# Performance work log

Measured on AMD Instinct MI355X. Metric: run time of the kernel, lower is better.

## Reference

```python
import jax, jax.numpy as jnp
import numpy as np
from jax import lax

PI = float(np.pi)
K_TOP = 128
N_BINS = 64

def _normalize(x, axis, eps=1e-12):
    n = jnp.sqrt(jnp.sum(x * x, axis=axis, keepdims=True))
    return x / jnp.maximum(n, eps)

def _conv(x, w, b):
    y = lax.conv_general_dilated(x, w, (1, 1), 'SAME',
                                 dimension_numbers=('NCHW', 'OIHW', 'NCHW'))
    return y + b[None, :, None, None]

def _maxpool2(x):
    return lax.reduce_window(x, -jnp.inf, lax.max, (1, 1, 2, 2), (1, 1, 2, 2), 'VALID')

def setup_inputs() -> dict:
    key = jax.random.key(0)
    ks = jax.random.split(key, 12)
    B, C, H, W = 16, 1, 512, 512
    PD, NPT = 128, 64
    fc_in = NPT + 64 * 4 * 4 + 3  # 1091
    def lin_init(k, fan_in, shape):
        bound = 1.0 / np.sqrt(fan_in)
        return jax.random.uniform(k, shape, jnp.float32, -bound, bound)
    return {
        'image': jax.random.normal(ks[0], (B, C, H, W), jnp.float32),
        'pattern_receptors': jax.random.normal(ks[1], (NPT, PD), jnp.float32) * 0.1,
        'conv1_w': lin_init(ks[2], 2 * 9, (32, 2, 3, 3)),
        'conv1_b': lin_init(ks[3], 2 * 9, (32,)),
        'conv2_w': lin_init(ks[4], 32 * 9, (64, 32, 3, 3)),
        'conv2_b': lin_init(ks[5], 32 * 9, (64,)),
        'fc1_w': lin_init(ks[6], fc_in, (512, fc_in)),
        'fc1_b': lin_init(ks[7], fc_in, (512,)),
        'fc2_w': lin_init(ks[8], 512, (PD, 512)),
        'fc2_b': lin_init(ks[9], 512, (PD,)),
        'ln_g': jnp.ones((PD,), jnp.float32),
        'ln_b': jnp.zeros((PD,), jnp.float32),
    }

def reference(image, pattern_receptors, conv1_w, conv1_b, conv2_w, conv2_b,
              fc1_w, fc1_b, fc2_w, fc2_b, ln_g, ln_b):
    B, C, H, W = image.shape
    # ---- frequency domain ----
    freq = jnp.fft.fft2(image, axes=(2, 3))
    magnitude = jnp.abs(freq)
    phase = jnp.angle(freq)
    # ---- pattern matching (topk of FFT magnitude vs receptor library) ----
    flat_mag = magnitude.reshape(B, C, -1)
    dom, _ = lax.top_k(flat_mag, K_TOP)          # [B, C, 128]
    dom = dom.reshape(B, -1)                     # [B, C*128]
    sims = jnp.matmul(_normalize(dom, 1), _normalize(pattern_receptors, 1).T)  # [B, 64]
    # ---- spatial path (original detaches via numpy roundtrip) ----
    img = lax.stop_gradient(image)
    gy = jnp.gradient(img, axis=2)
    gx = jnp.gradient(img, axis=3)
    gmag = jnp.sqrt(gx * gx + gy * gy)
    gori = jnp.arctan2(gy, gx)
    spat_in = jnp.stack([gmag, gori], axis=2).reshape(B, 2 * C, H, W)
    h = jax.nn.relu(_conv(spat_in, conv1_w, conv1_b))
    h = _maxpool2(h)                             # [B,32,H/2,W/2]
    h = jax.nn.relu(_conv(h, conv2_w, conv2_b))  # [B,64,H/2,W/2]
    Hp, Wp = h.shape[2], h.shape[3]
    h = h.reshape(B, 64, 4, Hp // 4, 4, Wp // 4).mean(axis=(3, 5))  # adaptive avg 4x4
    spatial = h.reshape(B, -1)                   # [B, 1024]
    # ---- phase statistics ----
    pf = phase.reshape(B, -1)
    p_mean = jnp.mean(pf, axis=1)
    p_std = jnp.std(pf, axis=1, ddof=1)
    bins = jnp.clip(jnp.floor((pf + PI) / (2 * PI) * N_BINS), 0, N_BINS - 1).astype(jnp.int32)
    hist = jnp.zeros((B, N_BINS), jnp.float32).at[jnp.arange(B)[:, None], bins].add(1.0)
    hist = hist / jnp.sum(hist, axis=1, keepdims=True)
    p_ent = -jnp.sum(hist * jnp.log(hist + 1e-10), axis=1)
    phase_feats = jnp.stack([p_mean, p_std, p_ent], axis=1)  # [B, 3]
    # ---- fuse: MLP + LayerNorm ----
    combined = jnp.concatenate([sims, spatial, phase_feats], axis=1)  # [B, 1091]
    z = jax.nn.relu(combined @ fc1_w.T + fc1_b)
    z = z @ fc2_w.T + fc2_b
    mu = jnp.mean(z, axis=-1, keepdims=True)
    var = jnp.var(z, axis=-1, keepdims=True)
    holo = (z - mu) / jnp.sqrt(var + 1e-5) * ln_g + ln_b
    return sims, spatial, phase_feats, holo
```

## Files before the change

### kernel.cpp

```cpp
#include <hip/hip_runtime.h>
#include <hip/hip_fp16.h>
#include <math.h>


#define PI_F 3.14159274f
#define TWO_PI_F 6.28318548f

typedef _Float16 half8 __attribute__((ext_vector_type(8)));
typedef _Float16 h2 __attribute__((ext_vector_type(2)));
typedef float floatx4 __attribute__((ext_vector_type(4)));

#define OFF_BIG   8388608
#define OFF_SMALL 25165824
#define NBIN 2048

__global__ void __launch_bounds__(256) init_kernel(float* __restrict__ zp,
                                                   float2* __restrict__ tw,
                                                   const float* __restrict__ w2,
                                                   const float* __restrict__ w1,
                                                   _Float16* __restrict__ wrep,
                                                   _Float16* __restrict__ w1r) {
    int idx = blockIdx.x * 256 + threadIdx.x;
    if (idx < 82992) zp[idx] = 0.0f;
    if (idx < 512) {
        if (idx == 0) tw[0] = make_float2(1.f, 0.f);
        else {
            int h = 31 - __clz(idx);
            int H = 1 << h;
            float sn, cs;
            sincosf(-PI_F * (float)(idx - H) / (float)H, &sn, &cs);
            tw[idx] = make_float2(cs, sn);
        }
    }
    if (idx < 18432) {
        int j = idx & 7;
        int lane = (idx >> 3) & 63;
        int nt = (idx >> 9) & 3;
        int tap = idx >> 11;
        int oc = nt * 16 + (lane & 15);
        int ic = (lane >> 4) * 8 + j;
        wrep[idx] = (_Float16)w2[(oc * 32 + ic) * 9 + tap];
    }
    if (idx < 1024) {
        int j = idx & 7;
        int lane = (idx >> 3) & 63;
        int nt = idx >> 9;
        int oc = nt * 16 + (lane & 15);
        int k = (lane >> 4) * 8 + j;
        _Float16 v = (_Float16)0.f;
        if (k < 18) {
            int tap = k >> 1, ch = k & 1;
            v = (_Float16)w1[oc * 18 + ch * 9 + tap];
        }
        w1r[idx] = v;
    }
}

__global__ void __launch_bounds__(256) fft_rows2(const float* __restrict__ img,
                                                 const float2* __restrict__ twg,
                                                 h2* __restrict__ rowhf) {
    __shared__ float2 s[512];
    __shared__ float2 tw[512];
    const int t = threadIdx.x;
    const long long rbase = (long long)blockIdx.x * 1024;
    const float* x0 = img + rbase;
    const float* x1 = x0 + 512;

    for (int i = t; i < 512; i += 256) tw[i] = twg[i];
    for (int i = t; i < 512; i += 256) s[i] = make_float2(x0[i], x1[i]);
    __syncthreads();
#pragma unroll
    for (int st = 9; st >= 1; --st) {
        const int half = 1 << (st - 1);
        const int pos = t & (half - 1);
        const int grp = t >> (st - 1);
        const int i1 = (grp << st) + pos;
        const int i2 = i1 + half;
        float2 w = tw[half + pos];
        float2 a = s[i1], b = s[i2];
        float dx = a.x - b.x, dy = a.y - b.y;
        s[i1] = make_float2(a.x + b.x, a.y + b.y);
        s[i2] = make_float2(dx * w.x - dy * w.y, dx * w.y + dy * w.x);
        __syncthreads();
    }
    for (int i = t; i < 512; i += 256) {
        int k = __brev((unsigned)i) >> 23;
        int kp = (512 - k) & 511;
        int jp = __brev((unsigned)kp) >> 23;
        float2 Z = s[i], Zp = s[jp];
        rowhf[rbase + i]       = h2{(_Float16)(0.5f * (Z.x + Zp.x)),
                                    (_Float16)(0.5f * (Z.y - Zp.y))};
        rowhf[rbase + 512 + i] = h2{(_Float16)(0.5f * (Z.y + Zp.y)),
                                    (_Float16)(-0.5f * (Z.x - Zp.x))};
    }
}

__global__ void __launch_bounds__(256) fft_cols(const h2* __restrict__ rowhf,
                                                const float2* __restrict__ twg,
                                                _Float16* __restrict__ magT,
                                                float* __restrict__ psum,
                                                float* __restrict__ psumsq,
                                                unsigned* __restrict__ phist,
                                                unsigned* __restrict__ mhist) {
    __shared__ float2 s[8 * 512];
    __shared__ float2 tw[512];
    __shared__ unsigned ph[64];
    __shared__ unsigned mh[NBIN];
    __shared__ float red[8];
    const int t = threadIdx.x;
    const int b = blockIdx.x >> 6;
    const int x0 = (blockIdx.x & 63) * 8;

    for (int i = t; i < 512; i += 256) tw[i] = twg[i];
    if (t < 64) ph[t] = 0u;
    for (int i = t; i < NBIN; i += 256) mh[i] = 0u;
    for (int idx = t; idx < 8 * 512; idx += 256) {
        int y = idx >> 3;
        int c = idx & 7;
        h2 v = rowhf[((long long)(b * 512 + y)) * 512 + x0 + c];
        s[c * 512 + y] = make_float2((float)v[0], (float)v[1]);
    }
    __syncthreads();

    const int c = t >> 5;
    const int j0 = t & 31;
    float2* sc = s + c * 512;
#pragma unroll
    for (int st = 9; st >= 1; --st) {
        const int half = 1 << (st - 1);
#pragma unroll
        for (int k = 0; k < 8; ++k) {
            int j = j0 + (k << 5);
            int pos = j & (half - 1);
            int grp = j >> (st - 1);
            int i1 = (grp << st) + pos;
            int i2 = i1 + half;
            float2 w = tw[half + pos];
            float2 a = sc[i1], bb = sc[i2];
            float dx = a.x - bb.x, dy = a.y - bb.y;
            sc[i1] = make_float2(a.x + bb.x, a.y + bb.y);
            sc[i2] = make_float2(dx * w.x - dy * w.y, dx * w.y + dy * w.x);
        }
        __syncthreads();
    }

    float lsum = 0.f, lsq = 0.f;
    for (int idx = t; idx < 8 * 512; idx += 256) {
        int cc = idx >> 9;
        int y = idx & 511;
        float2 v = s[cc * 512 + y];
        float mag = sqrtf(v.x * v.x + v.y * v.y);
        union { _Float16 h; unsigned short u; } cvt;
        cvt.h = (_Float16)mag;
        magT[((long long)(b * 512 + x0 + cc)) * 512 + y] = cvt.h;
        unsigned mb = min((unsigned)(cvt.u >> 4), (unsigned)(NBIN - 1));
        atomicAdd(&mh[mb], 1u);
        float phv = atan2f(v.y, v.x);
        lsum += phv;
        lsq += phv * phv;
        int bin = (int)floorf((phv + PI_F) / TWO_PI_F * 64.0f);
        bin = min(max(bin, 0), 63);
        atomicAdd(&ph[bin], 1u);
    }
    for (int off = 32; off > 0; off >>= 1) {
        lsum += __shfl_down(lsum, off);
        lsq  += __shfl_down(lsq, off);
    }
    if ((t & 63) == 0) { red[t >> 6] = lsum; red[4 + (t >> 6)] = lsq; }
    __syncthreads();
    if (t == 0) {
        atomicAdd(psum + b,   red[0] + red[1] + red[2] + red[3]);
        atomicAdd(psumsq + b, red[4] + red[5] + red[6] + red[7]);
    }
    if (t < 64 && ph[t]) atomicAdd(&phist[b * 64 + t], ph[t]);
    for (int i = t; i < NBIN; i += 256)
        if (mh[i]) atomicAdd(&mhist[b * NBIN + i], mh[i]);
}

__global__ void __launch_bounds__(256) thresh_kernel(const unsigned* __restrict__ mhist,
                                                     int* __restrict__ selbin) {
    __shared__ unsigned csum[256];
    const int b = blockIdx.x, t = threadIdx.x;
    unsigned s = 0;
    for (int i = 0; i < NBIN / 256; ++i) s += mhist[b * NBIN + t * (NBIN / 256) + i];
    csum[t] = s;
    __syncthreads();
    if (t == 0) {
        unsigned acc = 0; int chunk = 0;
        for (int i = 255; i >= 0; --i) {
            acc += csum[i];
            if (acc >= 128u) { chunk = i; break; }
        }
        unsigned acc2 = acc - csum[chunk];
        int tb = chunk * (NBIN / 256);
        for (int i = chunk * (NBIN / 256) + (NBIN / 256) - 1; i >= chunk * (NBIN / 256); --i) {
            acc2 += mhist[b * NBIN + i];
            if (acc2 >= 128u) { tb = i; break; }
        }
        selbin[b] = tb;
    }
}

#define TK_CAP 4096
__global__ void __launch_bounds__(256) collect_kernel(const _Float16* __restrict__ magT,
                                                      const int* __restrict__ selbin,
                                                      float* __restrict__ cand,
                                                      unsigned* __restrict__ ccnt) {
    const int blk = blockIdx.x;
    const int b = blk >> 4, chunk = blk & 15;
    const unsigned tb = (unsigned)selbin[b];
    const uint4* m = (const uint4*)(magT + (size_t)b * 262144 + chunk * 16384);
    float* cb = cand + b * TK_CAP;
    for (int i = threadIdx.x; i < 2048; i += 256) {
        uint4 v4 = m[i];
        unsigned vv[4] = {v4.x, v4.y, v4.z, v4.w};
#pragma unroll
        for (int j = 0; j < 4; ++j) {
#pragma unroll
            for (int k = 0; k < 2; ++k) {
                unsigned short ub = (k == 0) ? (unsigned short)(vv[j] & 0xFFFFu)
                                             : (unsigned short)(vv[j] >> 16);
                if ((unsigned)(ub >> 4) >= tb) {
                    unsigned p = atomicAdd(&ccnt[b], 1u);
                    if (p < TK_CAP) {
                        union { unsigned short u; _Float16 h; } c2;
                        c2.u = ub;
                        cb[p] = (float)c2.h;
                    }
                }
            }
        }
    }
}

__global__ void __launch_bounds__(1024) sort_kernel(const float* __restrict__ cand,
                                                    const unsigned* __restrict__ ccnt,
                                                    float* __restrict__ dom) {
    __shared__ float c[TK_CAP];
    const int b = blockIdx.x, t = threadIdx.x;
    const unsigned n = min(ccnt[b], (unsigned)TK_CAP);
    int P = 256;
    while (P < (int)n) P <<= 1;
    for (int i = t; i < P; i += 1024) c[i] = (i < (int)n) ? cand[b * TK_CAP + i] : -1.0f;
    __syncthreads();
    for (int k = 2; k <= P; k <<= 1) {
        for (int j = k >> 1; j > 0; j >>= 1) {
            for (int i = t; i < P; i += 1024) {
                int ixj = i ^ j;
                if (ixj > i) {
                    float a = c[i], d = c[ixj];
                    bool up = ((i & k) == 0);
                    if (up ? (a < d) : (a > d)) { c[i] = d; c[ixj] = a; }
                }
            }
            __syncthreads();
        }
    }
    if (t < 128) dom[b * 128 + t] = c[t];
}

__global__ void __launch_bounds__(256) sims_kernel(const float* __restrict__ dom,
                                                   const float* __restrict__ rec,
                                                   float* __restrict__ comb,
                                                   float* __restrict__ dout) {
    __shared__ float sd[16 * 128];
    __shared__ float sr[64 * 128];
    __shared__ float scale[80];
    const int t = threadIdx.x;
    for (int i = t; i < 2048; i += 256) sd[i] = dom[i];
    for (int i = t; i < 8192; i += 256) sr[i] = rec[i];
    __syncthreads();
    if (t < 80) {
        const float* base = (t < 16) ? (sd + t * 128) : (sr + (t - 16) * 128);
        float s = 0.f;
        for (int k = 0; k < 128; ++k) s += base[k] * base[k];
        scale[t] = 1.0f / fmaxf(sqrtf(s), 1e-12f);
    }
    __syncthreads();
    for (int o = t; o < 1024; o += 256) {
        int b = o >> 6, p = o & 63;
        const float* dv = sd + b * 128;
        const float* rv = sr + p * 128;
        float s = 0.f;
        for (int k = 0; k < 128; ++k) s += dv[k] * rv[k];
        float val = s * scale[b] * scale[16 + p];
        dout[b * 64 + p] = val;
        comb[b * 1091 + p] = val;
    }
}

__global__ void __launch_bounds__(256) grad_conv1_mfma(const float* __restrict__ img,
                                                       const half8* __restrict__ w1r,
                                                       const float* __restrict__ c1b,
                                                       _Float16* __restrict__ h1) {
    __shared__ float simg[36 * 37];
    __shared__ _Float16 sgrad[(34 * 36 + 1) * 2];
    const int blk = blockIdx.x;
    const int b = blk >> 8;
    const int tr = blk & 255;
    const int TY = (tr >> 4) * 32, TX = (tr & 15) * 32;
    const int t = threadIdx.x;
    const float* im = img + (long long)b * 262144;

    for (int idx = t; idx < 1296; idx += 256) {
        int iy = idx / 36, ix = idx - iy * 36;
        int gy = min(max(TY - 2 + iy, 0), 511);
        int gx = min(max(TX - 2 + ix, 0), 511);
        simg[iy * 37 + ix] = im[gy * 512 + gx];
    }
    if (t == 0) { sgrad[2448] = (_Float16)0.f; sgrad[2449] = (_Float16)0.f; }
    __syncthreads();

    for (int idx = t; idx < 1156; idx += 256) {
        int ly = idx / 34, lx = idx - ly * 34;
        int gy = TY - 1 + ly, gx = TX - 1 + lx;
        float up = simg[ly * 37 + lx + 1];
        float dn = simg[(ly + 2) * 37 + lx + 1];
        float lf = simg[(ly + 1) * 37 + lx];
        float rt = simg[(ly + 1) * 37 + lx + 2];
        float fy = (gy <= 0 || gy >= 511) ? 1.f : 0.5f;
        float fx = (gx <= 0 || gx >= 511) ? 1.f : 0.5f;
        float gyv = (dn - up) * fy, gxv = (rt - lf) * fx;
        bool inside = ((unsigned)gy < 512u) && ((unsigned)gx < 512u);
        float mag = inside ? sqrtf(gxv * gxv + gyv * gyv) : 0.f;
        float ori = inside ? atan2f(gyv, gxv) : 0.f;
        int p = (ly * 36 + lx) * 2;
        sgrad[p] = (_Float16)mag;
        sgrad[p + 1] = (_Float16)ori;
    }
    __syncthreads();

    const int w = t >> 6, lane = t & 63;
    const int q = lane >> 4, m = lane & 15;
    const int oc0 = m, oc1 = 16 + m;
    const float bias0 = c1b[oc0], bias1 = c1b[oc1];
    half8 Bf0 = w1r[lane], Bf1 = w1r[64 + lane];
    const unsigned* gp = (const unsigned*)sgrad;
    const int ZP = 1224;

    const int sy = (m >> 1) & 1, sx = m & 1, dqx = m >> 2;

#pragma unroll 4
    for (int i = 0; i < 16; ++i) {
        const int mt = w * 16 + i;
        const int qy = mt >> 2, qxg = mt & 3;
        const int py = 2 * qy + sy;
        const int px = 2 * (qxg * 4 + dqx) + sx;
        const int base = py * 36 + px;

        int o0 = (q == 0) ? base      : (q == 1) ? base + 37 : (q == 2) ? base + 74 : ZP;
        int o1 = (q == 0) ? base + 1  : (q == 1) ? base + 38 : ZP;
        int o2 = (q == 0) ? base + 2  : (q == 1) ? base + 72 : ZP;
        int o3 = (q == 0) ? base + 36 : (q == 1) ? base + 73 : ZP;

        union { unsigned u[4]; half8 h; } Af;
        Af.u[0] = gp[o0]; Af.u[1] = gp[o1]; Af.u[2] = gp[o2]; Af.u[3] = gp[o3];

        floatx4 acc0 = {bias0, bias0, bias0, bias0};
        floatx4 acc1 = {bias1, bias1, bias1, bias1};
        acc0 = __builtin_amdgcn_mfma_f32_16x16x32_f16(Af.h, Bf0, acc0, 0, 0, 0);
        acc1 = __builtin_amdgcn_mfma_f32_16x16x32_f16(Af.h, Bf1, acc1, 0, 0, 0);

        float v0 = fmaxf(fmaxf(acc0[0], acc0[1]), fmaxf(acc0[2], acc0[3]));
        float v1 = fmaxf(fmaxf(acc1[0], acc1[1]), fmaxf(acc1[2], acc1[3]));
        v0 = fmaxf(v0, 0.f);
        v1 = fmaxf(v1, 0.f);

        const int PY = (TY >> 1) + qy;
        const int PX = (TX >> 1) + qxg * 4 + q;
        _Float16* dst = h1 + (((size_t)(b * 256 + PY)) * 256 + PX) * 32;
        dst[oc0] = (_Float16)v0;
        dst[oc1] = (_Float16)v1;
    }
}

__global__ void __launch_bounds__(256) conv2_mfma(const _Float16* __restrict__ h1,
                                                  const _Float16* __restrict__ wrep,
                                                  const float* __restrict__ c2b,
                                                  float* __restrict__ sacc) {
    __shared__ _Float16 tile[18 * 34 * 32];
    __shared__ float lsum[64];
    const int blk = blockIdx.x;
    const int b  = blk >> 7;
    const int yt = (blk >> 3) & 15;
    const int xt = blk & 7;
    const int y0 = yt * 16, x0 = xt * 32;
    const int t = threadIdx.x;
    if (t < 64) lsum[t] = 0.f;

    for (int c = t; c < 18 * 136; c += 256) {
        int row = c / 136;
        int chunk = c - row * 136;
        int gy = y0 - 1 + row;
        int px = chunk >> 2;
        int gx = x0 - 1 + px;
        floatx4 v = {0.f, 0.f, 0.f, 0.f};
        if ((unsigned)gy < 256u && (unsigned)gx < 256u)
            v = *(const floatx4*)(h1 + (((size_t)(b * 256 + gy)) * 256 + gx) * 32 + (chunk & 3) * 8);
        *(floatx4*)(tile + (row * 34 + px) * 32 + (chunk & 3) * 8) = v;
    }
    __syncthreads();

    const int w = t >> 6, lane = t & 63;
    const int q = lane >> 4, ln15 = lane & 15;
    float bias[4];
#pragma unroll
    for (int nt = 0; nt < 4; ++nt) bias[nt] = c2b[nt * 16 + ln15];
    float partial[4] = {0.f, 0.f, 0.f, 0.f};

#pragma unroll 1
    for (int gr = 0; gr < 2; ++gr) {
        floatx4 acc[4][4];
#pragma unroll
        for (int mt = 0; mt < 4; ++mt)
#pragma unroll
            for (int nt = 0; nt < 4; ++nt)
                acc[mt][nt] = floatx4{bias[nt], bias[nt], bias[nt], bias[nt]};

        const _Float16* ab = tile + (((w * 4 + gr * 2) * 34) + ln15) * 32 + q * 8;
        const _Float16* wk = wrep + lane * 8;

#pragma unroll 1
        for (int ky = 0; ky < 3; ++ky) {
#pragma unroll
            for (int kx = 0; kx < 3; ++kx) {
                half8 Bf[4];
#pragma unroll
                for (int nt = 0; nt < 4; ++nt)
                    Bf[nt] = *(const half8*)(wk + (kx * 4 + nt) * 512);
#pragma unroll
                for (int mt = 0; mt < 4; ++mt) {
                    half8 Af = *(const half8*)(ab + (mt >> 1) * 1088 + (mt & 1) * 512 + kx * 32);
#pragma unroll
                    for (int nt = 0; nt < 4; ++nt)
                        acc[mt][nt] = __builtin_amdgcn_mfma_f32_16x16x32_f16(Af, Bf[nt], acc[mt][nt], 0, 0, 0);
                }
            }
            ab += 34 * 32;
            wk += 3 * 2048;
        }

#pragma unroll
        for (int mt = 0; mt < 4; ++mt)
#pragma unroll
            for (int nt = 0; nt < 4; ++nt)
#pragma unroll
                for (int rg = 0; rg < 4; ++rg)
                    partial[nt] += fmaxf(acc[mt][nt][rg], 0.f);
    }

#pragma unroll
    for (int nt = 0; nt < 4; ++nt) {
        float v = partial[nt];
        v += __shfl_xor(v, 16);
        v += __shfl_xor(v, 32);
        if (lane < 16) atomicAdd(&lsum[nt * 16 + ln15], v);
    }
    __syncthreads();
    const int cell = (yt >> 2) * 4 + (xt >> 1);
    if (t < 64) atomicAdd(&sacc[(((b << 6) + t) << 4) + cell], lsum[t]);
}

__global__ void __launch_bounds__(256) finalize_kernel(const float* __restrict__ sacc,
                                                       const float* __restrict__ psum,
                                                       const float* __restrict__ psumsq,
                                                       const unsigned* __restrict__ phist,
                                                       float* __restrict__ comb,
                                                       float* __restrict__ dout) {
    if (blockIdx.x < 64) {
        int idx = blockIdx.x * 256 + threadIdx.x;
        int b = idx >> 10, j = idx & 1023;
        float v = sacc[idx] * (1.0f / 4096.0f);
        dout[1024 + idx] = v;
        comb[b * 1091 + 64 + j] = v;
    } else {
        int t = threadIdx.x;
        if (t < 16) {
            const float N = 262144.f;
            float s = psum[t];
            float mean = s / N;
            float var = (psumsq[t] - s * s / N) / (N - 1.f);
            float sd = sqrtf(fmaxf(var, 0.f));
            float ent = 0.f;
            for (int i = 0; i < 64; ++i) {
                float p = (float)phist[t * 64 + i] / N;
                ent -= p * logf(p + 1e-10f);
            }
            dout[17408 + t * 3 + 0] = mean;
            dout[17408 + t * 3 + 1] = sd;
            dout[17408 + t * 3 + 2] = ent;
            float* cb = comb + t * 1091 + 1088;
            cb[0] = mean; cb[1] = sd; cb[2] = ent;
        }
    }
}

__global__ void __launch_bounds__(256) fc1_kernel(const float* __restrict__ comb,
                                                  const float* __restrict__ W1,
                                                  const float* __restrict__ B1,
                                                  float* __restrict__ out1) {
    const int wid = blockIdx.x * 4 + (threadIdx.x >> 6);
    const int lane = threadIdx.x & 63;
    const int b = wid >> 9, o = wid & 511;
    const float* w = W1 + (size_t)o * 1091;
    const float* c = comb + b * 1091;
    float acc = 0.f;
#pragma unroll 4
    for (int i = 0; i < 17; ++i) {
        int k = i * 64 + lane;
        acc += w[k] * c[k];
    }
    if (lane < 3) acc += w[1088 + lane] * c[1088 + lane];
#pragma unroll
    for (int off = 32; off > 0; off >>= 1) acc += __shfl_down(acc, off);
    if (lane == 0) out1[b * 512 + o] = fmaxf(acc + B1[o], 0.f);
}

__global__ void __launch_bounds__(256) fc2_kernel(const float* __restrict__ out1,
                                                  const float* __restrict__ W2,
                                                  const float* __restrict__ B2,
                                                  float* __restrict__ z) {
    const int wid = blockIdx.x * 4 + (threadIdx.x >> 6);
    const int lane = threadIdx.x & 63;
    const int b = wid >> 7, o = wid & 127;
    const float* w = W2 + (size_t)o * 512;
    const float* c = out1 + b * 512;
    float acc = 0.f;
#pragma unroll
    for (int i = 0; i < 8; ++i) {
        int k = i * 64 + lane;
        acc += w[k] * c[k];
    }
#pragma unroll
    for (int off = 32; off > 0; off >>= 1) acc += __shfl_down(acc, off);
    if (lane == 0) z[b * 128 + o] = acc + B2[o];
}

__global__ void __launch_bounds__(128) ln_kernel(const float* __restrict__ z,
                                                 const float* __restrict__ g,
                                                 const float* __restrict__ beta,
                                                 float* __restrict__ dout) {
    __shared__ float red[4];
    const int b = blockIdx.x, t = threadIdx.x;
    float acc = z[b * 128 + t];
    float s = acc;
    for (int off = 32; off > 0; off >>= 1) s += __shfl_down(s, off);
    if ((t & 63) == 0) red[t >> 6] = s;
    __syncthreads();
    float mu = (red[0] + red[1]) * (1.0f / 128.0f);
    float d = acc - mu;
    float q = d * d;
    for (int off = 32; off > 0; off >>= 1) q += __shfl_down(q, off);
    if ((t & 63) == 0) red[2 + (t >> 6)] = q;
    __syncthreads();
    float var = (red[2] + red[3]) * (1.0f / 128.0f);
    dout[17456 + b * 128 + t] = d / sqrtf(var + 1e-5f) * g[t] + beta[t];
}

extern "C" void kernel_launch(void* const* d_in, const int* in_sizes, int n_in,
                              void* d_out, int out_size, void* d_ws, size_t ws_size,
                              hipStream_t stream) {
    const float* img = (const float*)d_in[0];
    const float* rec = (const float*)d_in[1];
    const float* w1  = (const float*)d_in[2];
    const float* c1b = (const float*)d_in[3];
    const float* w2  = (const float*)d_in[4];
    const float* c2b = (const float*)d_in[5];
    const float* fw1 = (const float*)d_in[6];
    const float* fb1 = (const float*)d_in[7];
    const float* fw2 = (const float*)d_in[8];
    const float* fb2 = (const float*)d_in[9];
    const float* lng = (const float*)d_in[10];
    const float* lnb = (const float*)d_in[11];
    float* out = (float*)d_out;

    float* ws = (float*)d_ws;
    h2* rowhf       = (h2*)ws;
    _Float16* magT  = (_Float16*)(ws + OFF_BIG);
    _Float16* h1    = (_Float16*)(ws + OFF_BIG);
    float* small_  = ws + OFF_SMALL;
    float* sacc    = small_;
    float* psum    = small_ + 16384;
    float* psumsq  = small_ + 16400;
    unsigned* phist = (unsigned*)(small_ + 16416);
    unsigned* mhist = (unsigned*)(small_ + 17440);
    unsigned* ccnt  = (unsigned*)(small_ + 82976);
    int* selbin    = (int*)(small_ + 82992);
    float* dom     = small_ + 83008;
    float* comb    = small_ + 85056;
    float* out1    = small_ + 102512;
    _Float16* wrep = (_Float16*)(small_ + 110704);
    float2* twg    = (float2*)(small_ + 119920);
    float* cand    = small_ + 120944;
    float* zbuf    = cand;
    _Float16* w1r  = (_Float16*)(small_ + 186480);

    init_kernel<<<325, 256, 0, stream>>>(sacc, twg, w2, w1, wrep, w1r);
    fft_rows2<<<4096, 256, 0, stream>>>(img, twg, rowhf);
    fft_cols<<<1024, 256, 0, stream>>>(rowhf, twg, magT, psum, psumsq, phist, mhist);
    thresh_kernel<<<16, 256, 0, stream>>>(mhist, selbin);
    collect_kernel<<<256, 256, 0, stream>>>(magT, selbin, cand, ccnt);
    sort_kernel<<<16, 1024, 0, stream>>>(cand, ccnt, dom);
    sims_kernel<<<1, 256, 0, stream>>>(dom, rec, comb, out);
    grad_conv1_mfma<<<4096, 256, 0, stream>>>(img, (const half8*)w1r, c1b, h1);
    conv2_mfma<<<2048, 256, 0, stream>>>(h1, wrep, c2b, sacc);
    finalize_kernel<<<65, 256, 0, stream>>>(sacc, psum, psumsq, phist, comb, out);
    fc1_kernel<<<2048, 256, 0, stream>>>(comb, fw1, fb1, out1);
    fc2_kernel<<<512, 256, 0, stream>>>(out1, fw2, fb2, zbuf);
    ln_kernel<<<16, 128, 0, stream>>>(zbuf, lng, lnb, out);
}
```

Before: 297.7 us.

## Register-resident column FFT with wave shuffles; pack conv1 output channel pairs

The column FFT now processes 16 columns per 512-thread block. Each 32-lane group holds 16 values of one column in registers. It does the first four radix-2 stages in registers and the last five with cross-lane shuffles, which removes the nine shared-memory passes and block barriers per stage. Shared staging is kept as half2 to shrink LDS. Separately, conv1 weights are reordered so each lane produces adjacent output channels, letting the output be written as one packed half2 store instead of two scalar stores. Register pressure grows (16 float2 per thread) and occupancy may change with 512-thread blocks.

Result: faster. 279.5 us (-6.1%).

```diff
diff --git a/kernel.cpp b/kernel.cpp
--- a/kernel.cpp
+++ b/kernel.cpp
@@ -45,7 +45,7 @@
         int j = idx & 7;
         int lane = (idx >> 3) & 63;
         int nt = idx >> 9;
-        int oc = nt * 16 + (lane & 15);
+        int oc = 2 * (lane & 15) + nt;
         int k = (lane >> 4) * 8 + j;
         _Float16 v = (_Float16)0.f;
         if (k < 18) {
@@ -95,85 +95,127 @@
     }
 }
 
-__global__ void __launch_bounds__(256) fft_cols(const h2* __restrict__ rowhf,
+#define FCOLS 16
+__global__ void __launch_bounds__(512) fft_cols(const h2* __restrict__ rowhf,
                                                 const float2* __restrict__ twg,
                                                 _Float16* __restrict__ magT,
                                                 float* __restrict__ psum,
                                                 float* __restrict__ psumsq,
                                                 unsigned* __restrict__ phist,
                                                 unsigned* __restrict__ mhist) {
-    __shared__ float2 s[8 * 512];
+    __shared__ h2 sh[FCOLS * 512];
     __shared__ float2 tw[512];
     __shared__ unsigned ph[64];
     __shared__ unsigned mh[NBIN];
-    __shared__ float red[8];
+    __shared__ float red[16];
     const int t = threadIdx.x;
-    const int b = blockIdx.x >> 6;
-    const int x0 = (blockIdx.x & 63) * 8;
-
-    for (int i = t; i < 512; i += 256) tw[i] = twg[i];
+    const int b = blockIdx.x >> 5;
+    const int x0 = (blockIdx.x & 31) * FCOLS;
+
+    for (int i = t; i < 512; i += 512) tw[i] = twg[i];
     if (t < 64) ph[t] = 0u;
-    for (int i = t; i < NBIN; i += 256) mh[i] = 0u;
-    for (int idx = t; idx < 8 * 512; idx += 256) {
-        int y = idx >> 3;
-        int c = idx & 7;
-        h2 v = rowhf[((long long)(b * 512 + y)) * 512 + x0 + c];
-        s[c * 512 + y] = make_float2((float)v[0], (float)v[1]);
+    for (int i = t; i < NBIN; i += 512) mh[i] = 0u;
+    for (int idx = t; idx < FCOLS * 512; idx += 512) {
+        int y = idx >> 4, c = idx & 15;
+        sh[c * 512 + y] = rowhf[((size_t)(b * 512 + y)) * 512 + x0 + c];
     }
     __syncthreads();
 
     const int c = t >> 5;
-    const int j0 = t & 31;
-    float2* sc = s + c * 512;
-#pragma unroll
-    for (int st = 9; st >= 1; --st) {
-        const int half = 1 << (st - 1);
-#pragma unroll
-        for (int k = 0; k < 8; ++k) {
-            int j = j0 + (k << 5);
-            int pos = j & (half - 1);
-            int grp = j >> (st - 1);
-            int i1 = (grp << st) + pos;
-            int i2 = i1 + half;
-            float2 w = tw[half + pos];
-            float2 a = sc[i1], bb = sc[i2];
+    const int j = t & 31;
+    float2 v[16];
+#pragma unroll
+    for (int r = 0; r < 16; ++r) {
+        h2 hv = sh[c * 512 + j + 32 * r];
+        v[r] = make_float2((float)hv[0], (float)hv[1]);
+    }
+#pragma unroll
+    for (int r = 0; r < 8; ++r) {
+        float2 w = tw[256 + j + 32 * r];
+        float2 a = v[r], bb = v[r + 8];
+        float dx = a.x - bb.x, dy = a.y - bb.y;
+        v[r]     = make_float2(a.x + bb.x, a.y + bb.y);
+        v[r + 8] = make_float2(dx * w.x - dy * w.y, dx * w.y + dy * w.x);
+    }
+#pragma unroll
+    for (int g = 0; g < 2; ++g)
+#pragma unroll
+        for (int rr = 0; rr < 4; ++rr) {
+            int r = g * 8 + rr;
+            float2 w = tw[128 + j + 32 * rr];
+            float2 a = v[r], bb = v[r + 4];
             float dx = a.x - bb.x, dy = a.y - bb.y;
-            sc[i1] = make_float2(a.x + bb.x, a.y + bb.y);
-            sc[i2] = make_float2(dx * w.x - dy * w.y, dx * w.y + dy * w.x);
-        }
-        __syncthreads();
+            v[r]     = make_float2(a.x + bb.x, a.y + bb.y);
+            v[r + 4] = make_float2(dx * w.x - dy * w.y, dx * w.y + dy * w.x);
+        }
+#pragma unroll
+    for (int g = 0; g < 4; ++g)
+#pragma unroll
+        for (int rr = 0; rr < 2; ++rr) {
+            int r = g * 4 + rr;
+            float2 w = tw[64 + j + 32 * rr];
+            float2 a = v[r], bb = v[r + 2];
+            float dx = a.x - bb.x, dy = a.y - bb.y;
+            v[r]     = make_float2(a.x + bb.x, a.y + bb.y);
+            v[r + 2] = make_float2(dx * w.x - dy * w.y, dx * w.y + dy * w.x);
+        }
+    {
+        float2 w = tw[32 + j];
+#pragma unroll
+        for (int g = 0; g < 8; ++g) {
+            int r = g * 2;
+            float2 a = v[r], bb = v[r + 1];
+            float dx = a.x - bb.x, dy = a.y - bb.y;
+            v[r]     = make_float2(a.x + bb.x, a.y + bb.y);
+            v[r + 1] = make_float2(dx * w.x - dy * w.y, dx * w.y + dy * w.x);
+        }
+    }
+#pragma unroll
+    for (int hs = 4; hs >= 0; --hs) {
+        const int h = 1 << hs;
+        float2 w = tw[h + (j & (h - 1))];
+        const bool upper = (j & h) != 0;
+#pragma unroll
+        for (int r = 0; r < 16; ++r) {
+            float ox = __shfl_xor(v[r].x, h);
+            float oy = __shfl_xor(v[r].y, h);
+            float sx = v[r].x + ox, sy = v[r].y + oy;
+            float dx = ox - v[r].x, dy = oy - v[r].y;
+            float tx = dx * w.x - dy * w.y, ty = dx * w.y + dy * w.x;
+            v[r].x = upper ? tx : sx;
+            v[r].y = upper ? ty : sy;
+        }
     }
 
     float lsum = 0.f, lsq = 0.f;
-    for (int idx = t; idx < 8 * 512; idx += 256) {
-        int cc = idx >> 9;
-        int y = idx & 511;
-        float2 v = s[cc * 512 + y];
-        float mag = sqrtf(v.x * v.x + v.y * v.y);
+    _Float16* mcol = magT + ((size_t)(b * 512 + x0 + c)) * 512;
+#pragma unroll
+    for (int r = 0; r < 16; ++r) {
+        float mag = sqrtf(v[r].x * v[r].x + v[r].y * v[r].y);
         union { _Float16 h; unsigned short u; } cvt;
         cvt.h = (_Float16)mag;
-        magT[((long long)(b * 512 + x0 + cc)) * 512 + y] = cvt.h;
-        unsigned mb = min((unsigned)(cvt.u >> 4), (unsigned)(NBIN - 1));
-        atomicAdd(&mh[mb], 1u);
-        float phv = atan2f(v.y, v.x);
+        mcol[j + 32 * r] = cvt.h;
+        atomicAdd(&mh[min((unsigned)(cvt.u >> 4), (unsigned)(NBIN - 1))], 1u);
+        float phv = atan2f(v[r].y, v[r].x);
         lsum += phv;
         lsq += phv * phv;
-        int bin = (int)floorf((phv + PI_F) / TWO_PI_F * 64.0f);
-        bin = min(max(bin, 0), 63);
+        int bin = min(max((int)floorf((phv + PI_F) / TWO_PI_F * 64.0f), 0), 63);
         atomicAdd(&ph[bin], 1u);
     }
     for (int off = 32; off > 0; off >>= 1) {
         lsum += __shfl_down(lsum, off);
         lsq  += __shfl_down(lsq, off);
     }
-    if ((t & 63) == 0) { red[t >> 6] = lsum; red[4 + (t >> 6)] = lsq; }
+    if ((t & 63) == 0) { red[t >> 6] = lsum; red[8 + (t >> 6)] = lsq; }
     __syncthreads();
     if (t == 0) {
-        atomicAdd(psum + b,   red[0] + red[1] + red[2] + red[3]);
-        atomicAdd(psumsq + b, red[4] + red[5] + red[6] + red[7]);
+        float s = 0.f, q = 0.f;
+        for (int i = 0; i < 8; ++i) { s += red[i]; q += red[8 + i]; }
+        atomicAdd(psum + b, s);
+        atomicAdd(psumsq + b, q);
     }
     if (t < 64 && ph[t]) atomicAdd(&phist[b * 64 + t], ph[t]);
-    for (int i = t; i < NBIN; i += 256)
+    for (int i = t; i < NBIN; i += 512)
         if (mh[i]) atomicAdd(&mhist[b * NBIN + i], mh[i]);
 }
 
@@ -332,7 +374,7 @@
 
     const int w = t >> 6, lane = t & 63;
     const int q = lane >> 4, m = lane & 15;
-    const int oc0 = m, oc1 = 16 + m;
+    const int oc0 = 2 * m, oc1 = 2 * m + 1;
     const float bias0 = c1b[oc0], bias1 = c1b[oc1];
     half8 Bf0 = w1r[lane], Bf1 = w1r[64 + lane];
     const unsigned* gp = (const unsigned*)sgrad;
@@ -369,8 +411,7 @@
         const int PY = (TY >> 1) + qy;
         const int PX = (TX >> 1) + qxg * 4 + q;
         _Float16* dst = h1 + (((size_t)(b * 256 + PY)) * 256 + PX) * 32;
-        dst[oc0] = (_Float16)v0;
-        dst[oc1] = (_Float16)v1;
+        *(h2*)(dst + oc0) = h2{(_Float16)v0, (_Float16)v1};
     }
 }
 
@@ -597,7 +638,7 @@
 
     init_kernel<<<325, 256, 0, stream>>>(sacc, twg, w2, w1, wrep, w1r);
     fft_rows2<<<4096, 256, 0, stream>>>(img, twg, rowhf);
-    fft_cols<<<1024, 256, 0, stream>>>(rowhf, twg, magT, psum, psumsq, phist, mhist);
+    fft_cols<<<512, 512, 0, stream>>>(rowhf, twg, magT, psum, psumsq, phist, mhist);
     thresh_kernel<<<16, 256, 0, stream>>>(mhist, selbin);
     collect_kernel<<<256, 256, 0, stream>>>(magT, selbin, cand, ccnt);
     sort_kernel<<<16, 1024, 0, stream>>>(cand, ccnt, dom);
```
